# Kernel tuning notes

Measured on AMD Instinct MI355X. Metric: run time of the kernel, lower is better.

The kernel has to match this reference:

```python
import jax, jax.numpy as jnp
import numpy as np
from jax import lax

VOXEL = 0.4
PC_START = np.array([-75.2, -75.2], dtype=np.float32)
GAMMA = 1.0
IOU_THRESH = 0.5


def setup_inputs() -> dict:
    key = jax.random.key(0)
    k1, k2, k3, k4, k5, k6, k7, k8 = jax.random.split(key, 8)
    N, M = 200000, 128
    xy = jax.random.uniform(k1, (N, 2), minval=-75.0, maxval=75.0)
    z = jax.random.uniform(k2, (N, 1), minval=-2.0, maxval=4.0)
    feat = jax.random.normal(k3, (N, 2))
    points = jnp.concatenate([xy, z, feat], axis=-1)            # [N,5]
    centers = jax.random.uniform(k4, (M, 2), minval=-70.0, maxval=70.0)
    cz = jax.random.uniform(k5, (M, 1), minval=-1.0, maxval=2.0)
    dims = jax.random.uniform(k6, (M, 3), minval=1.0, maxval=5.0)
    head = jax.random.uniform(k7, (M, 1), minval=-3.14, maxval=3.14)
    boxes = jnp.concatenate([centers, cz, dims, head], axis=-1)  # [M,7]
    labels = jax.random.randint(k8, (M,), 0, 3, dtype=jnp.int32)
    return {"points": points, "boxes": boxes, "labels": labels,
            "num_sample": 256, "num_anchors": 3}


def reference(points, boxes, labels, num_sample, num_anchors):
    # points: [N,5] (x,y,z,feat,feat); boxes: [M,7] (x,y,z,dx,dy,dz,heading)
    M = boxes.shape[0]
    pc_start = jnp.asarray(PC_START)

    # ---- voxel radius query (static-shape: boolean mask instead of compaction) ----
    coords = jnp.floor((points[:, :2] - pc_start) / VOXEL)          # [N,2]
    qcoords = jnp.floor((boxes[:, :2] - pc_start) / VOXEL)          # [M,2]
    rad_vox = jnp.ceil(jnp.linalg.norm(boxes[:, 3:5] / 2, axis=-1) * GAMMA / VOXEL)  # [M]
    dist = jnp.abs(qcoords[:, None, :] - coords[None, :, :])        # [M,N,2]
    vmask = jnp.any(jnp.all(dist < rad_vox[:, None, None], axis=-1), axis=0)  # [N]

    # ---- point-in-circle masks (cylindrical pool) ----
    radii = jnp.linalg.norm(boxes[:, 3:5] / 2, axis=-1) * GAMMA     # [M]
    dis = jnp.linalg.norm(points[None, :, :2] - boxes[:, None, :2], axis=-1)  # [M,N]
    point_mask = (dis <= radii[:, None]) & vmask[None, :]           # [M,N] bool
    pmf = point_mask.astype(jnp.float32)

    # ---- mask-IoU between same-class boxes (calculate_miou_gpu) ----
    inter = pmf @ pmf.T                                             # [M,M]
    cnt = pmf.sum(-1)
    union = cnt[:, None] + cnt[None, :] - inter
    same = labels[:, None] == labels[None, :]
    eye = jnp.eye(M, dtype=bool)
    miou = jnp.where(same & (~eye) & (union > 0), inter / jnp.maximum(union, 1.0), 0.0)
    miou_max = miou.max(-1)
    miou_idx = jnp.argmax(miou, -1)

    # ---- sequential greedy anchor grouping (sample_anchor) ----
    def step(carry, i):
        aidx, gof, gcnt, ng = carry
        j = miou_idx[i]
        gj = gof[j]
        gjs = jnp.maximum(gj, 0)
        join = (miou_max[i] > IOU_THRESH) & (gj >= 0) & (gcnt[gjs] < num_anchors)
        tg = jnp.where(join, gjs, ng)
        ts = jnp.where(join, gcnt[gjs], 0)
        aidx = aidx.at[tg, ts].set(i)
        gof = gof.at[i].set(tg)
        gcnt = gcnt.at[tg].add(1)
        ng = ng + jnp.where(join, 0, 1)
        return (aidx, gof, gcnt, ng), None

    init = (jnp.full((M, num_anchors), -1, jnp.int32),
            jnp.full((M,), -1, jnp.int32),
            jnp.zeros((M,), jnp.int32),
            jnp.int32(0))
    (anchors_idx, _, _, _), _ = lax.scan(step, init, jnp.arange(M, dtype=jnp.int32))

    # ---- merge member masks into group-leader masks, topk + gather ----
    safe = jnp.maximum(anchors_idx, 0)                              # [M,A]
    slot_valid = (anchors_idx >= 0).astype(jnp.float32)             # [M,A]
    merged = jnp.einsum('ga,gan->gn', slot_valid, pmf[safe])        # [M,N]
    smask, sidx = lax.top_k(merged, num_sample)                     # [M,S]
    sampled = points[sidx]                                          # [M,S,5]
    group_valid = anchors_idx[:, 0] >= 0                            # [M]
    sampled = jnp.where((smask[..., None] > 0) & group_valid[:, None, None], sampled, 0.0)
    return sampled, anchors_idx
```

## Files before the change

kernel.cpp:

```cpp
#pragma clang fp contract(off)
#include <hip/hip_runtime.h>
#include <hip/hip_bf16.h>

typedef unsigned long long u64;
typedef unsigned int u32;

#define NPTS   200000
#define MBOX   128
#define W64    3125
#define W64C   3200
#define SSAMP  256
#define AANCH  3
#define VOXELF 0.4f
#define PCSF   -75.2f
#define TILEW  9.375f

__global__ __launch_bounds__(256) void kZP(uint4* __restrict__ zbase,
                                           const float* __restrict__ boxes,
                                           float* __restrict__ bpk,
                                           u64* __restrict__ tmask)
{
    int tid = threadIdx.x;
    zbase[(size_t)blockIdx.x * 256 + tid] = make_uint4(0, 0, 0, 0);
    if (blockIdx.x != 0) return;

    __shared__ float sbx[128], sby[128], srch[128];
    if (tid < 128) {
        float bx = boxes[tid*7+0], by = boxes[tid*7+1];
        float dx = boxes[tid*7+3], dy = boxes[tid*7+4];
        float hx = dx * 0.5f, hy = dy * 0.5f;
        float sq = hx*hx;
        sq = sq + hy*hy;
        float r = sqrtf(sq);
        float qx = floorf((bx - PCSF) / VOXELF);
        float qy = floorf((by - PCSF) / VOXELF);
        float rv = ceilf(r / VOXELF);
        bpk[tid*8+0] = bx; bpk[tid*8+1] = by; bpk[tid*8+2] = r;  bpk[tid*8+3] = qx;
        bpk[tid*8+4] = qy; bpk[tid*8+5] = rv; bpk[tid*8+6] = 0.f; bpk[tid*8+7] = 0.f;
        sbx[tid] = bx; sby[tid] = by;
        srch[tid] = VOXELF * (rv + 2.0f);
    }
    __syncthreads();
    int tx = tid & 15, ty = tid >> 4;
    float x0 = -75.0f + tx * TILEW, x1 = x0 + TILEW;
    float y0 = -75.0f + ty * TILEW, y1 = y0 + TILEW;
    u64 m0 = 0, m1 = 0;
    for (int m = 0; m < 128; ++m) {
        float rc = srch[m];
        bool c = (sbx[m] > x0 - rc) & (sbx[m] < x1 + rc) &
                 (sby[m] > y0 - rc) & (sby[m] < y1 + rc);
        if (m < 64) m0 |= ((u64)c) << m;
        else        m1 |= ((u64)c) << (m - 64);
    }
    tmask[tid*2]   = m0;
    tmask[tid*2+1] = m1;
}

__global__ __launch_bounds__(256) void kA(const float* __restrict__ points,
                                          const float* __restrict__ bpk,
                                          const u64* __restrict__ tmask,
                                          u64* __restrict__ rowbits,
                                          u32* __restrict__ inter)
{
    __shared__ float4 sB4[128];
    __shared__ float2 sB2[128];
    __shared__ u64 sTM[512];
    int tid = threadIdx.x;
    if (tid < 128) {
        const float4* bp = (const float4*)bpk;
        float4 a = bp[tid*2];
        float4 b = bp[tid*2+1];
        sB4[tid] = a;
        sB2[tid] = make_float2(b.x, b.y);
    }
    sTM[tid]       = tmask[tid];
    sTM[tid + 256] = tmask[tid + 256];
    __syncthreads();

    int n = blockIdx.x * 256 + tid;
    if (n >= NPTS) return;
    float px = points[n*5+0], py = points[n*5+1];
    float cxn = floorf((px - PCSF) / VOXELF);
    float cyn = floorf((py - PCSF) / VOXELF);
    int tx = (int)floorf((px + 75.0f) * (1.0f / TILEW));
    int ty = (int)floorf((py + 75.0f) * (1.0f / TILEW));
    tx = tx < 0 ? 0 : (tx > 15 ? 15 : tx);
    ty = ty < 0 ? 0 : (ty > 15 ? 15 : ty);
    int tile = ty * 16 + tx;
    u64 c0 = sTM[tile*2], c1 = sTM[tile*2+1];
    u64 h0 = 0, h1 = 0;
    bool voxany = false;
    while (c0) {
        int m = __builtin_ctzll(c0); c0 &= c0 - 1;
        float4 bd = sB4[m]; float2 be = sB2[m];
        float ddx = px - bd.x, ddy = py - bd.y;
        float sq = ddx*ddx;
        sq = sq + ddy*ddy;
        float dis = sqrtf(sq);
        bool hit = (dis <= bd.z);
        bool vox = (fabsf(bd.w - cxn) < be.y) & (fabsf(be.x - cyn) < be.y);
        voxany |= vox;
        h0 |= ((u64)hit) << m;
    }
    while (c1) {
        int m = __builtin_ctzll(c1); c1 &= c1 - 1;
        float4 bd = sB4[m + 64]; float2 be = sB2[m + 64];
        float ddx = px - bd.x, ddy = py - bd.y;
        float sq = ddx*ddx;
        sq = sq + ddy*ddy;
        float dis = sqrtf(sq);
        bool hit = (dis <= bd.z);
        bool vox = (fabsf(bd.w - cxn) < be.y) & (fabsf(be.x - cyn) < be.y);
        voxany |= vox;
        h1 |= ((u64)hit) << m;
    }
    if (!voxany) { h0 = 0; h1 = 0; }
    if ((h0 | h1) == 0) return;

    int w = n >> 6, lane = n & 63;
    u64 lanebit = 1ull << lane;
    u64 e = h0;
    while (e) {
        int m = __builtin_ctzll(e); e &= e - 1;
        atomicOr(&rowbits[(size_t)m * W64C + w], lanebit);
        u64 f = h0;
        while (f) { int j = __builtin_ctzll(f); f &= f - 1; atomicAdd(&inter[m*128 + j], 1u); }
        f = h1;
        while (f) { int j = __builtin_ctzll(f); f &= f - 1; atomicAdd(&inter[m*128 + 64 + j], 1u); }
    }
    e = h1;
    while (e) {
        int m = __builtin_ctzll(e); e &= e - 1;
        atomicOr(&rowbits[(size_t)(m + 64) * W64C + w], lanebit);
        u64 f = h0;
        while (f) { int j = __builtin_ctzll(f); f &= f - 1; atomicAdd(&inter[(m+64)*128 + j], 1u); }
        f = h1;
        while (f) { int j = __builtin_ctzll(f); f &= f - 1; atomicAdd(&inter[(m+64)*128 + 64 + j], 1u); }
    }
}

__global__ __launch_bounds__(64) void kC1(const u32* __restrict__ inter,
                                          const int* __restrict__ labels,
                                          float* __restrict__ mmaxW,
                                          int* __restrict__ midxW)
{
    int i = blockIdx.x, lane = threadIdx.x;
    int j1 = lane, j2 = lane + 64;
    u32 ci = inter[i * 128 + i];
    int li = labels[i];
    u32 I1 = inter[i * 128 + j1];
    u32 I2 = inter[i * 128 + j2];
    u32 c1 = inter[j1 * 128 + j1];
    u32 c2 = inter[j2 * 128 + j2];
    int l1 = labels[j1], l2 = labels[j2];
    long un1 = (long)ci + (long)c1 - (long)I1;
    long un2 = (long)ci + (long)c2 - (long)I2;
    float v1 = 0.0f, v2 = 0.0f;
    if ((j1 != i) && (l1 == li) && (un1 > 0))
        v1 = (float)I1 / fmaxf((float)un1, 1.0f);
    if ((j2 != i) && (l2 == li) && (un2 > 0))
        v2 = (float)I2 / fmaxf((float)un2, 1.0f);
    float vm = fmaxf(v1, v2);
    #pragma unroll
    for (int d = 1; d < 64; d <<= 1)
        vm = fmaxf(vm, __shfl_xor(vm, d));
    u64 b1 = __ballot(v1 == vm);
    u64 b2 = __ballot(v2 == vm);
    int j = b1 ? __builtin_ctzll(b1) : 64 + __builtin_ctzll(b2);
    if (lane == 0) { mmaxW[i] = vm; midxW[i] = j; }
}

__global__ __launch_bounds__(256) void kD(const float* __restrict__ mmaxW,
                                          const int* __restrict__ midxW,
                                          const int* __restrict__ pNA,
                                          const u64* __restrict__ rowbits,
                                          const float* __restrict__ points,
                                          float* __restrict__ out,
                                          float* __restrict__ out_anchor)
{
    __shared__ float sMax[128];
    __shared__ int   sMidx[128];
    __shared__ int   sA[384];
    __shared__ int   sGof[128];
    __shared__ int   sCnt[128];
    __shared__ u64   sStat[2];
    __shared__ int   sNA;
    __shared__ u32   sl3[256], sl2[256], sl1[256];
    __shared__ u64   swt[13][4];
    int tid = threadIdx.x, bid = blockIdx.x;
    int lane = tid & 63, wv = tid >> 6;

    if (tid < 128) {
        sMax[tid]  = mmaxW[tid];
        sMidx[tid] = midxW[tid];
        sA[tid] = -1; sA[tid + 128] = -1; sA[tid + 256] = -1;
    }
    if (tid == 255) sNA = *pNA;
    __syncthreads();
    if (wv == 0) {
        bool st1 = (sMax[lane] <= 0.5f)      || (sMidx[lane] >= lane);
        bool st2 = (sMax[lane + 64] <= 0.5f) || (sMidx[lane + 64] >= lane + 64);
        u64 b1 = __ballot(st1);
        u64 b2 = __ballot(st2);
        if (lane == 0) { sStat[0] = b1; sStat[1] = b2; }
    }
    __syncthreads();
    if (tid == 0) {
        int NA = sNA;
        u64 st0 = sStat[0], st1 = sStat[1];
        int ng = 0;
        for (int i = 0; i < 128; ++i) {
            bool isStatic = (i < 64) ? ((st0 >> i) & 1ull) : ((st1 >> (i - 64)) & 1ull);
            if (isStatic) {
                sA[ng * AANCH] = i;
                sGof[i] = ng;
                sCnt[ng] = 1;
                ng++;
            } else {
                int j  = sMidx[i];
                int gj = sGof[j];
                int gc = sCnt[gj];
                if (gc < NA) {
                    sA[gj * AANCH + gc] = i;
                    sGof[i] = gj;
                    sCnt[gj] = gc + 1;
                } else {
                    sA[ng * AANCH] = i;
                    sGof[i] = ng;
                    sCnt[ng] = 1;
                    ng++;
                }
            }
        }
    }
    __syncthreads();
    if (bid == 0) {
        for (int t = tid; t < 384; t += 256)
            out_anchor[t] = (float)sA[t];
    }

    int g = bid;
    float* outg = out + (size_t)g * SSAMP * 5;
    int a0 = sA[g*3+0], a1 = sA[g*3+1], a2 = sA[g*3+2];
    if (a0 < 0) {
        for (int t = tid; t < SSAMP * 5; t += 256) outg[t] = 0.0f;
        return;
    }
    bool vB = (a1 >= 0), vC = (a2 >= 0);
    const u64* rA = rowbits + (size_t)a0 * W64C;
    const u64* rB = rowbits + (size_t)(vB ? a1 : 0) * W64C;
    const u64* rC = rowbits + (size_t)(vC ? a2 : 0) * W64C;
    const u64 M21 = (1ull << 21) - 1;

    u64 va[13], vb[13], vc[13];
    #pragma unroll
    for (int k = 0; k < 13; ++k) {
        int w = k * 256 + tid;
        bool inr = (w < W64);
        va[k] = inr ? rA[w] : 0ull;
        vb[k] = (inr && vB) ? rB[w] : 0ull;
        vc[k] = (inr && vC) ? rC[w] : 0ull;
    }
    u64 exl[13];
    #pragma unroll
    for (int k = 0; k < 13; ++k) {
        u64 a = va[k], b = vb[k], c = vc[k];
        u64 m3 = a & b & c;
        u64 any2 = (a & b) | (a & c) | (b & c);
        u64 m2 = any2 & ~m3;
        u64 m1 = (a | b | c) & ~any2;
        u64 own = ((u64)__popcll(m3) << 42) | ((u64)__popcll(m2) << 21) | (u64)__popcll(m1);
        u64 p = own;
        #pragma unroll
        for (int d = 1; d < 64; d <<= 1) {
            u64 t = __shfl_up(p, d);
            if (lane >= d) p += t;
        }
        if (lane == 63) swt[k][wv] = p;
        exl[k] = p - own;
    }
    __syncthreads();
    u64 base = 0;
    #pragma unroll
    for (int k = 0; k < 13; ++k) {
        u64 off = base + exl[k];
        for (int w2 = 0; w2 < wv; ++w2) off += swt[k][w2];
        u64 a = va[k], b = vb[k], c = vc[k];
        u64 m3 = a & b & c;
        u64 any2 = (a & b) | (a & c) | (b & c);
        u64 m2 = any2 & ~m3;
        u64 m1 = (a | b | c) & ~any2;
        u32 e3 = (u32)(off >> 42);
        u32 e2 = (u32)((off >> 21) & M21);
        u32 e1 = (u32)(off & M21);
        int nb = k * 256 * 64 + tid * 64;
        u64 mm = m3; u32 o = e3;
        while (mm) { int b2 = __builtin_ctzll(mm); mm &= mm - 1; if (o < 256) sl3[o] = nb + b2; o++; }
        mm = m2; o = e2;
        while (mm) { int b2 = __builtin_ctzll(mm); mm &= mm - 1; if (o < 256) sl2[o] = nb + b2; o++; }
        mm = m1; o = e1;
        while (mm) { int b2 = __builtin_ctzll(mm); mm &= mm - 1; if (o < 256) sl1[o] = nb + b2; o++; }
        base += swt[k][0] + swt[k][1] + swt[k][2] + swt[k][3];
    }
    __syncthreads();
    u32 t3 = (u32)(base >> 42), t2c = (u32)((base >> 21) & M21), t1 = (u32)(base & M21);
    u32 s = (u32)tid;
    int n = -1;
    if (s < t3)                  n = (int)sl3[s];
    else if (s < t3 + t2c)       n = (int)sl2[s - t3];
    else if (s < t3 + t2c + t1)  n = (int)sl1[s - t3 - t2c];
    float v0=0.f, v1=0.f, v2=0.f, v3=0.f, v4=0.f;
    if (n >= 0) {
        const float* pp = points + (size_t)n * 5;
        v0 = pp[0]; v1 = pp[1]; v2 = pp[2]; v3 = pp[3]; v4 = pp[4];
    }
    outg[s*5+0] = v0; outg[s*5+1] = v1; outg[s*5+2] = v2;
    outg[s*5+3] = v3; outg[s*5+4] = v4;
}

extern "C" void kernel_launch(void* const* d_in, const int* in_sizes, int n_in,
                              void* d_out, int out_size, void* d_ws, size_t ws_size,
                              hipStream_t stream)
{
    const float* points = (const float*)d_in[0];
    const float* boxes  = (const float*)d_in[1];
    const int*   labels = (const int*)d_in[2];
    const int*   pNA    = (const int*)d_in[4];
    float* out = (float*)d_out;
    char* ws = (char*)d_ws;

    size_t rowsz = (size_t)MBOX * W64C * 8;
    u64*  rowbits = (u64*)ws;
    u32*  inter   = (u32*)(ws + rowsz);
    float* bpk    = (float*)(ws + rowsz + 65536);
    u64*  tmask   = (u64*)(ws + rowsz + 65536 + 4096);
    float* mmaxW  = (float*)(ws + rowsz + 65536 + 8192);
    int*   midxW  = (int*)(ws + rowsz + 65536 + 8704);

    float* out_anchor = out + (size_t)MBOX * SSAMP * 5;

    kZP<<<816, 256, 0, stream>>>((uint4*)ws, boxes, bpk, tmask);
    kA<<<(NPTS + 255) / 256, 256, 0, stream>>>(points, bpk, tmask, rowbits, inter);
    kC1<<<MBOX, 64, 0, stream>>>(inter, labels, mmaxW, midxW);
    kD<<<MBOX, 256, 0, stream>>>(mmaxW, midxW, pNA, rowbits, points, out, out_anchor);
}
```

Before: 51.82 us.

## Write rowbits via wave ballot transpose, fuse IoU argmax into kD, shrink zeroing

kA now builds each 64-bit row word with a ballot-based transpose across the wave and stores it directly. This replaces per-hit atomicOr and means the rowbits buffer no longer needs zeroing, so the zero kernel only clears the intersection matrix (16 blocks instead of 816). The separate kC1 IoU-argmax kernel is folded into kD: every block loads the full inter matrix into padded shared memory and computes the per-box best match, which removes one launch. In exchange, every kA thread now runs 128 ballots even when it has no hits, and every kD block repeats the IoU computation redundantly.

```diff
diff --git a/kernel.cpp b/kernel.cpp
--- a/kernel.cpp
+++ b/kernel.cpp
@@ -14,14 +14,15 @@
 #define VOXELF 0.4f
 #define PCSF   -75.2f
 #define TILEW  9.375f
-
-__global__ __launch_bounds__(256) void kZP(uint4* __restrict__ zbase,
-                                           const float* __restrict__ boxes,
-                                           float* __restrict__ bpk,
-                                           u64* __restrict__ tmask)
+#define PADW   129
+
+__global__ __launch_bounds__(256) void kZ(uint4* __restrict__ interZ,
+                                          const float* __restrict__ boxes,
+                                          float* __restrict__ bpk,
+                                          u64* __restrict__ tmask)
 {
     int tid = threadIdx.x;
-    zbase[(size_t)blockIdx.x * 256 + tid] = make_uint4(0, 0, 0, 0);
+    interZ[blockIdx.x * 256 + tid] = make_uint4(0, 0, 0, 0);
     if (blockIdx.x != 0) return;
 
     __shared__ float sbx[128], sby[128], srch[128];
@@ -115,14 +116,24 @@
         h1 |= ((u64)hit) << m;
     }
     if (!voxany) { h0 = 0; h1 = 0; }
+
+    int w = n >> 6, lane = n & 63;
+    u64 mylo = 0, myhi = 0;
+    for (int m = 0; m < 64; ++m) {
+        u64 bal = __ballot(((h0 >> m) & 1ull) != 0);
+        if (lane == m) mylo = bal;
+    }
+    for (int m = 0; m < 64; ++m) {
+        u64 bal = __ballot(((h1 >> m) & 1ull) != 0);
+        if (lane == m) myhi = bal;
+    }
+    rowbits[(size_t)lane * W64C + w]        = mylo;
+    rowbits[(size_t)(lane + 64) * W64C + w] = myhi;
+
     if ((h0 | h1) == 0) return;
-
-    int w = n >> 6, lane = n & 63;
-    u64 lanebit = 1ull << lane;
     u64 e = h0;
     while (e) {
         int m = __builtin_ctzll(e); e &= e - 1;
-        atomicOr(&rowbits[(size_t)m * W64C + w], lanebit);
         u64 f = h0;
         while (f) { int j = __builtin_ctzll(f); f &= f - 1; atomicAdd(&inter[m*128 + j], 1u); }
         f = h1;
@@ -131,7 +142,6 @@
     e = h1;
     while (e) {
         int m = __builtin_ctzll(e); e &= e - 1;
-        atomicOr(&rowbits[(size_t)(m + 64) * W64C + w], lanebit);
         u64 f = h0;
         while (f) { int j = __builtin_ctzll(f); f &= f - 1; atomicAdd(&inter[(m+64)*128 + j], 1u); }
         f = h1;
@@ -139,45 +149,17 @@
     }
 }
 
-__global__ __launch_bounds__(64) void kC1(const u32* __restrict__ inter,
+__global__ __launch_bounds__(256) void kD(const u32* __restrict__ inter,
                                           const int* __restrict__ labels,
-                                          float* __restrict__ mmaxW,
-                                          int* __restrict__ midxW)
-{
-    int i = blockIdx.x, lane = threadIdx.x;
-    int j1 = lane, j2 = lane + 64;
-    u32 ci = inter[i * 128 + i];
-    int li = labels[i];
-    u32 I1 = inter[i * 128 + j1];
-    u32 I2 = inter[i * 128 + j2];
-    u32 c1 = inter[j1 * 128 + j1];
-    u32 c2 = inter[j2 * 128 + j2];
-    int l1 = labels[j1], l2 = labels[j2];
-    long un1 = (long)ci + (long)c1 - (long)I1;
-    long un2 = (long)ci + (long)c2 - (long)I2;
-    float v1 = 0.0f, v2 = 0.0f;
-    if ((j1 != i) && (l1 == li) && (un1 > 0))
-        v1 = (float)I1 / fmaxf((float)un1, 1.0f);
-    if ((j2 != i) && (l2 == li) && (un2 > 0))
-        v2 = (float)I2 / fmaxf((float)un2, 1.0f);
-    float vm = fmaxf(v1, v2);
-    #pragma unroll
-    for (int d = 1; d < 64; d <<= 1)
-        vm = fmaxf(vm, __shfl_xor(vm, d));
-    u64 b1 = __ballot(v1 == vm);
-    u64 b2 = __ballot(v2 == vm);
-    int j = b1 ? __builtin_ctzll(b1) : 64 + __builtin_ctzll(b2);
-    if (lane == 0) { mmaxW[i] = vm; midxW[i] = j; }
-}
-
-__global__ __launch_bounds__(256) void kD(const float* __restrict__ mmaxW,
-                                          const int* __restrict__ midxW,
                                           const int* __restrict__ pNA,
                                           const u64* __restrict__ rowbits,
                                           const float* __restrict__ points,
                                           float* __restrict__ out,
                                           float* __restrict__ out_anchor)
 {
+    __shared__ u32   sInt[128 * PADW];
+    __shared__ int   sLab[128];
+    __shared__ u64   sKey[128][2];
     __shared__ float sMax[128];
     __shared__ int   sMidx[128];
     __shared__ int   sA[384];
@@ -190,13 +172,52 @@
     int tid = threadIdx.x, bid = blockIdx.x;
     int lane = tid & 63, wv = tid >> 6;
 
+    {
+        const uint4* ip = (const uint4*)inter;
+        #pragma unroll
+        for (int k = 0; k < 16; ++k) {
+            uint4 v = ip[k * 256 + tid];
+            int e = (k * 256 + tid) * 4;
+            int row = e >> 7, col = e & 127;
+            u32* d = &sInt[row * PADW + col];
+            d[0] = v.x; d[1] = v.y; d[2] = v.z; d[3] = v.w;
+        }
+    }
     if (tid < 128) {
-        sMax[tid]  = mmaxW[tid];
-        sMidx[tid] = midxW[tid];
+        sLab[tid] = labels[tid];
         sA[tid] = -1; sA[tid + 128] = -1; sA[tid + 256] = -1;
     }
     if (tid == 255) sNA = *pNA;
     __syncthreads();
+
+    {
+        int r = tid >> 1, h = tid & 1;
+        u32 ci = sInt[r * PADW + r];
+        int li = sLab[r];
+        float best = 0.0f; int bj = h * 64;
+        #pragma unroll 4
+        for (int c = 0; c < 64; ++c) {
+            int j = h * 64 + c;
+            u32 I  = sInt[r * PADW + j];
+            u32 cj = sInt[j * PADW + j];
+            long un = (long)ci + (long)cj - (long)I;
+            float v = 0.0f;
+            if ((j != r) && (sLab[j] == li) && (un > 0))
+                v = (float)I / fmaxf((float)un, 1.0f);
+            if (v > best) { best = v; bj = j; }
+        }
+        sKey[r][h] = ((u64)__float_as_uint(best) << 32) | (u32)bj;
+    }
+    __syncthreads();
+    if (tid < 128) {
+        u64 k0 = sKey[tid][0], k1 = sKey[tid][1];
+        u32 v0 = (u32)(k0 >> 32), v1 = (u32)(k1 >> 32);
+        u64 kk = (v1 > v0) ? k1 : k0;
+        sMax[tid]  = __uint_as_float((u32)(kk >> 32));
+        sMidx[tid] = (int)(kk & 0xffffffffu);
+    }
+    __syncthreads();
+
     if (wv == 0) {
         bool st1 = (sMax[lane] <= 0.5f)      || (sMidx[lane] >= lane);
         bool st2 = (sMax[lane + 64] <= 0.5f) || (sMidx[lane + 64] >= lane + 64);
@@ -334,13 +355,10 @@
     u32*  inter   = (u32*)(ws + rowsz);
     float* bpk    = (float*)(ws + rowsz + 65536);
     u64*  tmask   = (u64*)(ws + rowsz + 65536 + 4096);
-    float* mmaxW  = (float*)(ws + rowsz + 65536 + 8192);
-    int*   midxW  = (int*)(ws + rowsz + 65536 + 8704);
 
     float* out_anchor = out + (size_t)MBOX * SSAMP * 5;
 
-    kZP<<<816, 256, 0, stream>>>((uint4*)ws, boxes, bpk, tmask);
+    kZ<<<16, 256, 0, stream>>>((uint4*)inter, boxes, bpk, tmask);
     kA<<<(NPTS + 255) / 256, 256, 0, stream>>>(points, bpk, tmask, rowbits, inter);
-    kC1<<<MBOX, 64, 0, stream>>>(inter, labels, mmaxW, midxW);
-    kD<<<MBOX, 256, 0, stream>>>(mmaxW, midxW, pNA, rowbits, points, out, out_anchor);
+    kD<<<MBOX, 256, 0, stream>>>(inter, labels, pNA, rowbits, points, out, out_anchor);
 }
```

New measurement: 65.95 us. 27.3% more time.
